# Optimization experiments

Hardware: AMD Instinct MI355X
Metric: run time of the kernel (lower is better)

The kernel has to match this reference:

```python
import jax, jax.numpy as jnp
import numpy as np

S, N, H, AD, AR = 256, 1024, 512, 128, 2

def setup_inputs() -> dict:
    key = jax.random.key(0)
    k0, k1, k2, k3, k4, k5 = jax.random.split(key, 6)
    xav1 = np.sqrt(2.0 / (H + AD)).astype(np.float32)   # xavier_normal std for [H,AD]
    xav2 = np.sqrt(2.0 / (AD + AR)).astype(np.float32)  # xavier_normal std for [AD,AR]
    return {
        "pre_emb_padded": jax.random.normal(k0, (S, N, H), jnp.float32),
        "fol_emb_padded": jax.random.normal(k1, (S, N, H), jnp.float32),
        "pre_attn_mask": jnp.zeros((N, S), jnp.bool_),
        "fol_attn_mask": jnp.zeros((N, S), jnp.bool_),
        "pre_is_valid": jnp.ones((N,), jnp.int32),
        "fol_is_valid": jnp.ones((N,), jnp.int32),
        "W1_pre": jax.random.normal(k2, (H, AD), jnp.float32) * xav1,
        "W2_pre": jax.random.normal(k3, (AD, AR), jnp.float32) * xav2,
        "W1_fol": jax.random.normal(k4, (H, AD), jnp.float32) * xav1,
        "W2_fol": jax.random.normal(k5, (AD, AR), jnp.float32) * xav2,
    }

def _attn_pool(emb, mask, W1, W2):
    # emb: [S, N, H] -> x: [N, S, H]
    x = jnp.transpose(emb, (1, 0, 2))
    s = jnp.tanh(x @ W1) @ W2                 # [N, S, 2]
    s = jax.nn.softmax(s, axis=1)             # softmax over seq (first softmax)
    s = jnp.transpose(s, (0, 2, 1))           # [N, 2, S]
    s = jnp.where(mask[:, None, :], -jnp.inf, s)
    s = jax.nn.softmax(s, axis=-1)            # masked second softmax over seq
    return jnp.einsum('nrs,nsh->nrh', s, x)   # [N, 2, H]

def _scatter_valid(h, valid):
    # reproduce the python valid-list gather: valid rows take next chunk, else zeros
    pos = jnp.cumsum(valid) - 1               # [N]
    return jnp.where((valid > 0)[:, None, None], h[pos], jnp.zeros((), h.dtype))

def reference(pre_emb_padded, fol_emb_padded, pre_attn_mask, fol_attn_mask,
              pre_is_valid, fol_is_valid, W1_pre, W2_pre, W1_fol, W2_fol):
    h_pre = _scatter_valid(_attn_pool(pre_emb_padded, pre_attn_mask, W1_pre, W2_pre), pre_is_valid)
    h_fol = _scatter_valid(_attn_pool(fol_emb_padded, fol_attn_mask, W1_fol, W2_fol), fol_is_valid)
    # mean over the attn_r=2 rows, concat along feature dim -> [N, 1, 2H]
    return jnp.concatenate([h_pre.mean(axis=1, keepdims=True),
                            h_fol.mean(axis=1, keepdims=True)], axis=2)
```

## Files before the change

### kernel.cpp

```cpp
#include <hip/hip_runtime.h>
#include <hip/hip_bf16.h>
#include <cstdint>
#include <cstddef>

#define S_ 256
#define N_ 1024
#define H_ 512
#define AD_ 128
static constexpr int M_TOTAL = N_ * S_;

typedef __attribute__((ext_vector_type(8))) short short8;
typedef __attribute__((ext_vector_type(4))) float f32x4;

__device__ __forceinline__ short8 pack8(float4 a, float4 b) {
  union { short8 s; __hip_bfloat162 h[4]; } u;
  u.h[0] = __float22bfloat162_rn(make_float2(a.x, a.y));
  u.h[1] = __float22bfloat162_rn(make_float2(a.z, a.w));
  u.h[2] = __float22bfloat162_rn(make_float2(b.x, b.y));
  u.h[3] = __float22bfloat162_rn(make_float2(b.z, b.w));
  return u.s;
}

__global__ __launch_bounds__(256) void k_w1frag(
    const float* __restrict__ w1_pre, const float* __restrict__ w1_fol,
    unsigned short* __restrict__ w1f) {
  int idx = blockIdx.x * 256 + threadIdx.x;
  int st = blockIdx.y;
  const float* w1 = st ? w1_fol : w1_pre;
  int j = idx & 7;
  int lane = (idx >> 3) & 63;
  int c = (idx >> 9) & 7;
  int kk = idx >> 12;
  int k = kk * 32 + ((lane >> 4) << 3) + j;
  int d = c * 16 + (lane & 15);
  __hip_bfloat16 hb = __float2bfloat16(w1[(size_t)k * AD_ + d]);
  w1f[(size_t)st * 65536 + idx] = *(unsigned short*)&hb;
}

__global__ __launch_bounds__(1024) void k_scan(
    const int* __restrict__ valid_pre, const int* __restrict__ valid_fol,
    int* __restrict__ pos) {
  const int st = blockIdx.x;
  const int* valid = st ? valid_fol : valid_pre;
  __shared__ int buf[1024];
  const int t = threadIdx.x;
  buf[t] = valid[t];
  __syncthreads();
  for (int off = 1; off < 1024; off <<= 1) {
    int v = (t >= off) ? buf[t - off] : 0;
    __syncthreads();
    buf[t] += v;
    __syncthreads();
  }
  pos[st * N_ + t] = buf[t] - 1;
}

__global__ __launch_bounds__(512) void k_logits(
    const float* __restrict__ emb_pre, const float* __restrict__ emb_fol,
    const unsigned short* __restrict__ w1f,
    const float* __restrict__ w2_pre, const float* __restrict__ w2_fol,
    float* __restrict__ logits) {
  __shared__ __align__(16) unsigned short Bs[65536];

  const int bid = blockIdx.x;
  const int st = bid >> 10;
  const int m0 = (bid & 1023) * 256;
  const float* __restrict__ emb = st ? emb_fol : emb_pre;
  const float* __restrict__ w2  = st ? w2_fol : w2_pre;

  const int t = threadIdx.x;
  const int w = t >> 6, lane = t & 63;
  const int r16 = lane & 15, kq = lane >> 4;

  {
    const uint4* src = (const uint4*)(w1f + (size_t)st * 65536);
    uint4* dst = (uint4*)Bs;
#pragma unroll
    for (int i = 0; i < 16; ++i) dst[t + i * 512] = src[t + i * 512];
  }
  __syncthreads();

  const unsigned short* bb = Bs + lane * 8;

  const float* a0 = emb + (size_t)(m0 + w * 32 + r16) * H_ + kq * 8;

  f32x4 acc[2][8];
#pragma unroll
  for (int f = 0; f < 2; ++f)
#pragma unroll
    for (int c = 0; c < 8; ++c) acc[f][c] = (f32x4){0.f, 0.f, 0.f, 0.f};

  float4 xb[3][2][2];
#pragma unroll
  for (int p = 0; p < 3; ++p)
#pragma unroll
    for (int f = 0; f < 2; ++f) {
      const float* ap = a0 + f * (16 * H_) + p * 32;
      xb[p][f][0] = *(const float4*)ap;
      xb[p][f][1] = *(const float4*)(ap + 4);
    }

#pragma unroll
  for (int kk = 0; kk < 16; ++kk) {
    const int sl = kk % 3;
    short8 b[8];
    const unsigned short* bp = bb + kk * 4096;
#pragma unroll
    for (int c = 0; c < 8; ++c) b[c] = *(const short8*)(bp + c * 512);
    short8 af0 = pack8(xb[sl][0][0], xb[sl][0][1]);
    short8 af1 = pack8(xb[sl][1][0], xb[sl][1][1]);
    if (kk + 3 < 16) {
#pragma unroll
      for (int f = 0; f < 2; ++f) {
        const float* ap = a0 + f * (16 * H_) + (kk + 3) * 32;
        xb[sl][f][0] = *(const float4*)ap;
        xb[sl][f][1] = *(const float4*)(ap + 4);
      }
    }
#pragma unroll
    for (int c = 0; c < 8; ++c) {
      acc[0][c] = __builtin_amdgcn_mfma_f32_16x16x32_bf16(af0, b[c], acc[0][c], 0, 0, 0);
      acc[1][c] = __builtin_amdgcn_mfma_f32_16x16x32_bf16(af1, b[c], acc[1][c], 0, 0, 0);
    }
  }

  float w2v0[8], w2v1[8];
#pragma unroll
  for (int c = 0; c < 8; ++c) {
    w2v0[c] = w2[(c * 16 + r16) * 2 + 0];
    w2v1[c] = w2[(c * 16 + r16) * 2 + 1];
  }
#pragma unroll
  for (int f = 0; f < 2; ++f) {
#pragma unroll
    for (int q = 0; q < 4; ++q) {
      float p0 = 0.f, p1 = 0.f;
#pragma unroll
      for (int c = 0; c < 8; ++c) {
        float xc = fminf(fmaxf(acc[f][c][q], -10.f), 10.f);
        float e  = __expf(2.f * xc);
        float th = (e - 1.f) / (e + 1.f);
        p0 += th * w2v0[c];
        p1 += th * w2v1[c];
      }
      p0 += __shfl_xor(p0, 1); p0 += __shfl_xor(p0, 2);
      p0 += __shfl_xor(p0, 4); p0 += __shfl_xor(p0, 8);
      p1 += __shfl_xor(p1, 1); p1 += __shfl_xor(p1, 2);
      p1 += __shfl_xor(p1, 4); p1 += __shfl_xor(p1, 8);
      if (r16 == 0) {
        int m = m0 + w * 32 + f * 16 + kq * 4 + q;
        logits[((size_t)st * M_TOTAL + m) * 2 + 0] = p0;
        logits[((size_t)st * M_TOTAL + m) * 2 + 1] = p1;
      }
    }
  }
}

template <bool MAXRED>
__device__ __forceinline__ float blockRed(float v, float* buf) {
#pragma unroll
  for (int off = 32; off; off >>= 1) {
    float o = __shfl_xor(v, off);
    v = MAXRED ? fmaxf(v, o) : (v + o);
  }
  __syncthreads();
  if ((threadIdx.x & 63) == 0) buf[threadIdx.x >> 6] = v;
  __syncthreads();
  float r = buf[0];
#pragma unroll
  for (int i = 1; i < 4; ++i) r = MAXRED ? fmaxf(r, buf[i]) : (r + buf[i]);
  return r;
}

__global__ __launch_bounds__(256) void k_softmax(
    const float* __restrict__ logits,
    const unsigned char* __restrict__ mask_pre, const unsigned char* __restrict__ mask_fol,
    float* __restrict__ wbar) {
  const int n  = blockIdx.x;
  const int st = blockIdx.y;
  const unsigned char* mask = st ? mask_fol : mask_pre;
  const int s = threadIdx.x;

  float2 l = *(const float2*)&logits[((size_t)st * M_TOTAL + (size_t)s * N_ + n) * 2];
  const bool mk = mask[(size_t)n * S_ + s] != 0;

  __shared__ float buf[4];
  float q[2];
  float lv[2] = {l.x, l.y};
#pragma unroll
  for (int r = 0; r < 2; ++r) {
    float m1 = blockRed<true>(lv[r], buf);
    float e1 = __expf(lv[r] - m1);
    float s1 = blockRed<false>(e1, buf);
    float p1 = e1 / s1;
    float v  = mk ? -INFINITY : p1;
    float m2 = blockRed<true>(v, buf);
    float e2 = mk ? 0.f : __expf(v - m2);
    float s2 = blockRed<false>(e2, buf);
    q[r] = e2 / s2;
  }
  wbar[((size_t)st * N_ + n) * S_ + s] = 0.5f * (q[0] + q[1]);
}

__global__ __launch_bounds__(512) void k_pv2(
    const float* __restrict__ emb_pre, const float* __restrict__ emb_fol,
    const float* __restrict__ wbar,
    float* __restrict__ part) {
  const int bid = blockIdx.x;
  const int st  = bid >> 7;
  const int idx = bid & 127;
  const int nc  = idx >> 1;
  const int sh  = idx & 1;
  const int n0 = nc * 16, s0 = sh * 128;
  const float* __restrict__ emb = st ? emb_fol : emb_pre;

  const int t = threadIdx.x;
  const int nl = t >> 5;
  const int c0 = (t & 31) * 4;

  __shared__ float wl[16][128];
  for (int i = t; i < 2048; i += 512) {
    int j = i >> 7, sl = i & 127;
    wl[j][sl] = wbar[((size_t)st * N_ + n0 + j) * S_ + s0 + sl];
  }
  __syncthreads();

  float4 acc[4], cur[4], nxt[4];
#pragma unroll
  for (int j = 0; j < 4; ++j) acc[j] = (float4){0.f, 0.f, 0.f, 0.f};

  const float* rowp = emb + ((size_t)(s0 + 127) * N_ + n0 + nl) * H_ + c0;
  const size_t SSTR = (size_t)N_ * H_;
#pragma unroll
  for (int j = 0; j < 4; ++j) cur[j] = *(const float4*)(rowp + j * 128);

  for (int sl = 127; sl >= 0; --sl) {
    const float* nrow = rowp - SSTR;
    if (sl > 0) {
#pragma unroll
      for (int j = 0; j < 4; ++j) nxt[j] = *(const float4*)(nrow + j * 128);
    }
    const float wv = wl[nl][sl];
#pragma unroll
    for (int j = 0; j < 4; ++j) {
      acc[j].x += wv * cur[j].x;
      acc[j].y += wv * cur[j].y;
      acc[j].z += wv * cur[j].z;
      acc[j].w += wv * cur[j].w;
    }
#pragma unroll
    for (int j = 0; j < 4; ++j) cur[j] = nxt[j];
    rowp = nrow;
  }

  float* pp = part + (((size_t)(st * 2 + sh) * N_) + n0 + nl) * H_ + c0;
#pragma unroll
  for (int j = 0; j < 4; ++j) *(float4*)(pp + j * 128) = acc[j];
}

__global__ __launch_bounds__(256) void k_combine(
    const float* __restrict__ part, const int* __restrict__ pos,
    const int* __restrict__ valid_pre, const int* __restrict__ valid_fol,
    float* __restrict__ out) {
  const int n = blockIdx.x, t = threadIdx.x;
  const int st = t >> 7;
  const int c = (t & 127) * 4;
  const int* valid = st ? valid_fol : valid_pre;
  float4 r = {0.f, 0.f, 0.f, 0.f};
  if (valid[n] > 0) {
    int np = pos[st * N_ + n]; if (np < 0) np = 0;
    float4 a = *(const float4*)&part[(((size_t)(st * 2 + 0) * N_) + np) * H_ + c];
    float4 b = *(const float4*)&part[(((size_t)(st * 2 + 1) * N_) + np) * H_ + c];
    r.x = a.x + b.x; r.y = a.y + b.y; r.z = a.z + b.z; r.w = a.w + b.w;
  }
  *(float4*)&out[(size_t)n * 1024 + st * 512 + c] = r;
}

extern "C" void kernel_launch(void* const* d_in, const int* in_sizes, int n_in,
                              void* d_out, int out_size, void* d_ws, size_t ws_size,
                              hipStream_t stream) {
  const float* emb_pre = (const float*)d_in[0];
  const float* emb_fol = (const float*)d_in[1];
  const unsigned char* mask_pre = (const unsigned char*)d_in[2];
  const unsigned char* mask_fol = (const unsigned char*)d_in[3];
  const int* valid_pre = (const int*)d_in[4];
  const int* valid_fol = (const int*)d_in[5];
  const float* w1_pre = (const float*)d_in[6];
  const float* w2_pre = (const float*)d_in[7];
  const float* w1_fol = (const float*)d_in[8];
  const float* w2_fol = (const float*)d_in[9];
  float* out = (float*)d_out;

  char* ws = (char*)d_ws;
  unsigned short* w1f = (unsigned short*)ws;
  int*   pos    = (int*)(ws + 262144);
  float* logits = (float*)(ws + 270336);
  float* wbar   = (float*)(ws + 270336 + 4194304);
  float* part   = (float*)(ws + 270336 + 4194304 + 2097152);

  hipLaunchKernelGGL(k_w1frag, dim3(256, 2), dim3(256), 0, stream,
                     w1_pre, w1_fol, w1f);
  hipLaunchKernelGGL(k_scan, dim3(2), dim3(1024), 0, stream,
                     valid_pre, valid_fol, pos);
  hipLaunchKernelGGL(k_logits, dim3(2048), dim3(512), 0, stream,
                     emb_pre, emb_fol, w1f, w2_pre, w2_fol, logits);
  hipLaunchKernelGGL(k_softmax, dim3(N_, 2), dim3(256), 0, stream,
                     logits, mask_pre, mask_fol, wbar);
  hipLaunchKernelGGL(k_pv2, dim3(256), dim3(512), 0, stream,
                     emb_pre, emb_fol, wbar, part);
  hipLaunchKernelGGL(k_combine, dim3(N_), dim3(256), 0, stream,
                     part, pos, valid_pre, valid_fol, out);
}
```

Before: 455.4 us.

## Overlap pre-stream weighted pooling with fol-stream logits in one mixed launch

Splits the pipeline per stream: pre logits, pre softmax, then a combined kernel whose first 1024 blocks compute fol logits while the remaining 128 blocks do the pre weighted-sum pass, then fol softmax and fol pooling. The aim is to fill the GPU with low-occupancy pooling work (only 128 blocks per stream) alongside compute-heavy GEMM blocks instead of running them serially. The trade-off is more launches, and the mixed kernel reserves 128KB of shared memory for every block, including pooling blocks that need only 8KB, which limits how many fit per CU.

```diff
diff --git a/kernel.cpp b/kernel.cpp
--- a/kernel.cpp
+++ b/kernel.cpp
@@ -55,25 +55,15 @@
   pos[st * N_ + t] = buf[t] - 1;
 }
 
-__global__ __launch_bounds__(512) void k_logits(
-    const float* __restrict__ emb_pre, const float* __restrict__ emb_fol,
-    const unsigned short* __restrict__ w1f,
-    const float* __restrict__ w2_pre, const float* __restrict__ w2_fol,
-    float* __restrict__ logits) {
-  __shared__ __align__(16) unsigned short Bs[65536];
-
-  const int bid = blockIdx.x;
-  const int st = bid >> 10;
-  const int m0 = (bid & 1023) * 256;
-  const float* __restrict__ emb = st ? emb_fol : emb_pre;
-  const float* __restrict__ w2  = st ? w2_fol : w2_pre;
-
-  const int t = threadIdx.x;
+__device__ __forceinline__ void lg_body(
+    const float* __restrict__ emb, const unsigned short* __restrict__ w1f_st,
+    const float* __restrict__ w2, float* __restrict__ logits_st,
+    int m0, unsigned short* Bs, int t) {
   const int w = t >> 6, lane = t & 63;
   const int r16 = lane & 15, kq = lane >> 4;
 
   {
-    const uint4* src = (const uint4*)(w1f + (size_t)st * 65536);
+    const uint4* src = (const uint4*)w1f_st;
     uint4* dst = (uint4*)Bs;
 #pragma unroll
     for (int i = 0; i < 16; ++i) dst[t + i * 512] = src[t + i * 512];
@@ -81,7 +71,6 @@
   __syncthreads();
 
   const unsigned short* bb = Bs + lane * 8;
-
   const float* a0 = emb + (size_t)(m0 + w * 32 + r16) * H_ + kq * 8;
 
   f32x4 acc[2][8];
@@ -106,7 +95,7 @@
     short8 b[8];
     const unsigned short* bp = bb + kk * 4096;
 #pragma unroll
-    for (int c = 0; c < 8; ++c) b[c] = *(const short8*)(bp + c * 512);
+    for (int cc = 0; cc < 8; ++cc) b[cc] = *(const short8*)(bp + cc * 512);
     short8 af0 = pack8(xb[sl][0][0], xb[sl][0][1]);
     short8 af1 = pack8(xb[sl][1][0], xb[sl][1][1]);
     if (kk + 3 < 16) {
@@ -118,17 +107,17 @@
       }
     }
 #pragma unroll
-    for (int c = 0; c < 8; ++c) {
-      acc[0][c] = __builtin_amdgcn_mfma_f32_16x16x32_bf16(af0, b[c], acc[0][c], 0, 0, 0);
-      acc[1][c] = __builtin_amdgcn_mfma_f32_16x16x32_bf16(af1, b[c], acc[1][c], 0, 0, 0);
+    for (int cc = 0; cc < 8; ++cc) {
+      acc[0][cc] = __builtin_amdgcn_mfma_f32_16x16x32_bf16(af0, b[cc], acc[0][cc], 0, 0, 0);
+      acc[1][cc] = __builtin_amdgcn_mfma_f32_16x16x32_bf16(af1, b[cc], acc[1][cc], 0, 0, 0);
     }
   }
 
   float w2v0[8], w2v1[8];
 #pragma unroll
-  for (int c = 0; c < 8; ++c) {
-    w2v0[c] = w2[(c * 16 + r16) * 2 + 0];
-    w2v1[c] = w2[(c * 16 + r16) * 2 + 1];
+  for (int cc = 0; cc < 8; ++cc) {
+    w2v0[cc] = w2[(cc * 16 + r16) * 2 + 0];
+    w2v1[cc] = w2[(cc * 16 + r16) * 2 + 1];
   }
 #pragma unroll
   for (int f = 0; f < 2; ++f) {
@@ -136,12 +125,12 @@
     for (int q = 0; q < 4; ++q) {
       float p0 = 0.f, p1 = 0.f;
 #pragma unroll
-      for (int c = 0; c < 8; ++c) {
-        float xc = fminf(fmaxf(acc[f][c][q], -10.f), 10.f);
+      for (int cc = 0; cc < 8; ++cc) {
+        float xc = fminf(fmaxf(acc[f][cc][q], -10.f), 10.f);
         float e  = __expf(2.f * xc);
         float th = (e - 1.f) / (e + 1.f);
-        p0 += th * w2v0[c];
-        p1 += th * w2v1[c];
+        p0 += th * w2v0[cc];
+        p1 += th * w2v1[cc];
       }
       p0 += __shfl_xor(p0, 1); p0 += __shfl_xor(p0, 2);
       p0 += __shfl_xor(p0, 4); p0 += __shfl_xor(p0, 8);
@@ -149,10 +138,88 @@
       p1 += __shfl_xor(p1, 4); p1 += __shfl_xor(p1, 8);
       if (r16 == 0) {
         int m = m0 + w * 32 + f * 16 + kq * 4 + q;
-        logits[((size_t)st * M_TOTAL + m) * 2 + 0] = p0;
-        logits[((size_t)st * M_TOTAL + m) * 2 + 1] = p1;
+        logits_st[(size_t)m * 2 + 0] = p0;
+        logits_st[(size_t)m * 2 + 1] = p1;
       }
     }
+  }
+}
+
+__device__ __forceinline__ void pv_body(
+    const float* __restrict__ emb, const float* __restrict__ wbar_st,
+    float* __restrict__ part_st, int idx, float (*wl)[128], int t) {
+  const int nc = idx >> 1;
+  const int sh = idx & 1;
+  const int n0 = nc * 16, s0 = sh * 128;
+
+  const int nl = t >> 5;
+  const int c0 = (t & 31) * 4;
+
+  for (int i = t; i < 2048; i += 512) {
+    int j = i >> 7, sl = i & 127;
+    wl[j][sl] = wbar_st[(size_t)(n0 + j) * S_ + s0 + sl];
+  }
+  __syncthreads();
+
+  float4 acc[4], cur[4], nxt[4];
+#pragma unroll
+  for (int j = 0; j < 4; ++j) acc[j] = (float4){0.f, 0.f, 0.f, 0.f};
+
+  const float* rowp = emb + ((size_t)(s0 + 127) * N_ + n0 + nl) * H_ + c0;
+  const size_t SSTR = (size_t)N_ * H_;
+#pragma unroll
+  for (int j = 0; j < 4; ++j) cur[j] = *(const float4*)(rowp + j * 128);
+
+  for (int sl = 127; sl >= 0; --sl) {
+    const float* nrow = rowp - SSTR;
+    if (sl > 0) {
+#pragma unroll
+      for (int j = 0; j < 4; ++j) nxt[j] = *(const float4*)(nrow + j * 128);
+    }
+    const float wv = wl[nl][sl];
+#pragma unroll
+    for (int j = 0; j < 4; ++j) {
+      acc[j].x += wv * cur[j].x;
+      acc[j].y += wv * cur[j].y;
+      acc[j].z += wv * cur[j].z;
+      acc[j].w += wv * cur[j].w;
+    }
+#pragma unroll
+    for (int j = 0; j < 4; ++j) cur[j] = nxt[j];
+    rowp = nrow;
+  }
+
+  float* pp = part_st + ((size_t)sh * N_ + n0 + nl) * H_ + c0;
+#pragma unroll
+  for (int j = 0; j < 4; ++j) *(float4*)(pp + j * 128) = acc[j];
+}
+
+__global__ __launch_bounds__(512) void k_logits_s(
+    const float* __restrict__ emb, const unsigned short* __restrict__ w1f_st,
+    const float* __restrict__ w2, float* __restrict__ logits_st) {
+  __shared__ __align__(16) unsigned short Bs[65536];
+  lg_body(emb, w1f_st, w2, logits_st, blockIdx.x * 256, Bs, threadIdx.x);
+}
+
+__global__ __launch_bounds__(512) void k_pv_s(
+    const float* __restrict__ emb, const float* __restrict__ wbar_st,
+    float* __restrict__ part_st) {
+  __shared__ __align__(16) float wl[16][128];
+  pv_body(emb, wbar_st, part_st, blockIdx.x, wl, threadIdx.x);
+}
+
+__global__ __launch_bounds__(512) void k_mix(
+    const float* __restrict__ embB, const unsigned short* __restrict__ w1fB,
+    const float* __restrict__ w2B, float* __restrict__ logitsB,
+    const float* __restrict__ embA, const float* __restrict__ wbarA,
+    float* __restrict__ partA) {
+  __shared__ __align__(16) unsigned char smem[131072];
+  const int bid = blockIdx.x;
+  if (bid < 1024) {
+    lg_body(embB, w1fB, w2B, logitsB, bid * 256,
+            (unsigned short*)smem, threadIdx.x);
+  } else {
+    pv_body(embA, wbarA, partA, bid - 1024, (float(*)[128])smem, threadIdx.x);
   }
 }
 
@@ -172,17 +239,15 @@
   return r;
 }
 
-__global__ __launch_bounds__(256) void k_softmax(
-    const float* __restrict__ logits,
-    const unsigned char* __restrict__ mask_pre, const unsigned char* __restrict__ mask_fol,
-    float* __restrict__ wbar) {
-  const int n  = blockIdx.x;
-  const int st = blockIdx.y;
-  const unsigned char* mask = st ? mask_fol : mask_pre;
+__global__ __launch_bounds__(256) void k_softmax_s(
+    const float* __restrict__ logits_st,
+    const unsigned char* __restrict__ mask_st,
+    float* __restrict__ wbar_st) {
+  const int n = blockIdx.x;
   const int s = threadIdx.x;
 
-  float2 l = *(const float2*)&logits[((size_t)st * M_TOTAL + (size_t)s * N_ + n) * 2];
-  const bool mk = mask[(size_t)n * S_ + s] != 0;
+  float2 l = *(const float2*)&logits_st[((size_t)s * N_ + n) * 2];
+  const bool mk = mask_st[(size_t)n * S_ + s] != 0;
 
   __shared__ float buf[4];
   float q[2];
@@ -199,63 +264,7 @@
     float s2 = blockRed<false>(e2, buf);
     q[r] = e2 / s2;
   }
-  wbar[((size_t)st * N_ + n) * S_ + s] = 0.5f * (q[0] + q[1]);
-}
-
-__global__ __launch_bounds__(512) void k_pv2(
-    const float* __restrict__ emb_pre, const float* __restrict__ emb_fol,
-    const float* __restrict__ wbar,
-    float* __restrict__ part) {
-  const int bid = blockIdx.x;
-  const int st  = bid >> 7;
-  const int idx = bid & 127;
-  const int nc  = idx >> 1;
-  const int sh  = idx & 1;
-  const int n0 = nc * 16, s0 = sh * 128;
-  const float* __restrict__ emb = st ? emb_fol : emb_pre;
-
-  const int t = threadIdx.x;
-  const int nl = t >> 5;
-  const int c0 = (t & 31) * 4;
-
-  __shared__ float wl[16][128];
-  for (int i = t; i < 2048; i += 512) {
-    int j = i >> 7, sl = i & 127;
-    wl[j][sl] = wbar[((size_t)st * N_ + n0 + j) * S_ + s0 + sl];
-  }
-  __syncthreads();
-
-  float4 acc[4], cur[4], nxt[4];
-#pragma unroll
-  for (int j = 0; j < 4; ++j) acc[j] = (float4){0.f, 0.f, 0.f, 0.f};
-
-  const float* rowp = emb + ((size_t)(s0 + 127) * N_ + n0 + nl) * H_ + c0;
-  const size_t SSTR = (size_t)N_ * H_;
-#pragma unroll
-  for (int j = 0; j < 4; ++j) cur[j] = *(const float4*)(rowp + j * 128);
-
-  for (int sl = 127; sl >= 0; --sl) {
-    const float* nrow = rowp - SSTR;
-    if (sl > 0) {
-#pragma unroll
-      for (int j = 0; j < 4; ++j) nxt[j] = *(const float4*)(nrow + j * 128);
-    }
-    const float wv = wl[nl][sl];
-#pragma unroll
-    for (int j = 0; j < 4; ++j) {
-      acc[j].x += wv * cur[j].x;
-      acc[j].y += wv * cur[j].y;
-      acc[j].z += wv * cur[j].z;
-      acc[j].w += wv * cur[j].w;
-    }
-#pragma unroll
-    for (int j = 0; j < 4; ++j) cur[j] = nxt[j];
-    rowp = nrow;
-  }
-
-  float* pp = part + (((size_t)(st * 2 + sh) * N_) + n0 + nl) * H_ + c0;
-#pragma unroll
-  for (int j = 0; j < 4; ++j) *(float4*)(pp + j * 128) = acc[j];
+  wbar_st[(size_t)n * S_ + s] = 0.5f * (q[0] + q[1]);
 }
 
 __global__ __launch_bounds__(256) void k_combine(
@@ -298,16 +307,30 @@
   float* wbar   = (float*)(ws + 270336 + 4194304);
   float* part   = (float*)(ws + 270336 + 4194304 + 2097152);
 
+  const unsigned short* w1f_pre = w1f;
+  const unsigned short* w1f_fol = w1f + 65536;
+  float* logits_pre = logits;
+  float* logits_fol = logits + (size_t)M_TOTAL * 2;
+  float* wbar_pre = wbar;
+  float* wbar_fol = wbar + (size_t)N_ * S_;
+  float* part_pre = part;
+  float* part_fol = part + (size_t)2 * N_ * H_;
+
   hipLaunchKernelGGL(k_w1frag, dim3(256, 2), dim3(256), 0, stream,
                      w1_pre, w1_fol, w1f);
   hipLaunchKernelGGL(k_scan, dim3(2), dim3(1024), 0, stream,
                      valid_pre, valid_fol, pos);
-  hipLaunchKernelGGL(k_logits, dim3(2048), dim3(512), 0, stream,
-                     emb_pre, emb_fol, w1f, w2_pre, w2_fol, logits);
-  hipLaunchKernelGGL(k_softmax, dim3(N_, 2), dim3(256), 0, stream,
-                     logits, mask_pre, mask_fol, wbar);
-  hipLaunchKernelGGL(k_pv2, dim3(256), dim3(512), 0, stream,
-                     emb_pre, emb_fol, wbar, part);
+  hipLaunchKernelGGL(k_logits_s, dim3(1024), dim3(512), 0, stream,
+                     emb_pre, w1f_pre, w2_pre, logits_pre);
+  hipLaunchKernelGGL(k_softmax_s, dim3(N_), dim3(256), 0, stream,
+                     logits_pre, mask_pre, wbar_pre);
+  hipLaunchKernelGGL(k_mix, dim3(1152), dim3(512), 0, stream,
+                     emb_fol, w1f_fol, w2_fol, logits_fol,
+                     emb_pre, wbar_pre, part_pre);
+  hipLaunchKernelGGL(k_softmax_s, dim3(N_), dim3(256), 0, stream,
+                     logits_fol, mask_fol, wbar_fol);
+  hipLaunchKernelGGL(k_pv_s, dim3(128), dim3(512), 0, stream,
+                     emb_fol, wbar_fol, part_fol);
   hipLaunchKernelGGL(k_combine, dim3(N_), dim3(256), 0, stream,
                      part, pos, valid_pre, valid_fol, out);
 }
```

Result: slower. 473.4 us (+4.0%).
